# Kernel tuning notes

Hardware: AMD Instinct MI355X
Metric: run time of the kernel (lower is better)

## Reference

```python
import jax, jax.numpy as jnp
import numpy as np

MONOTONICITY = 1.0  # init kwarg monotonicity=1


def _interp_channel(xq, xs, ys):
    """Monotonic piecewise-linear interp for one channel.
    xq: (N,) query points; xs: (B,) sorted breakpoints; ys: (B,) knot values.
    Linear extrapolation beyond both ends using the edge segment slopes.
    """
    B = xs.shape[0]
    # segment index in [1, B-1]; elements below xs[0] / above xs[-1] use edge segments
    idx = jnp.clip(jnp.searchsorted(xs, xq), 1, B - 1)
    x0 = xs[idx - 1]
    x1 = xs[idx]
    y0 = ys[idx - 1]
    y1 = ys[idx]
    slope = (y1 - y0) / (x1 - x0)
    return y0 + slope * (xq - x0)


def setup_inputs() -> dict:
    key = jax.random.key(0)
    k1, k2, k3, k4 = jax.random.split(key, 4)
    N, C, B = 2097152, 16, 32
    x = jax.random.normal(k1, (N, C), dtype=jnp.float32)
    # learned parameters of MonoPointPWL (per channel)
    xp = jax.random.normal(k2, (C, B), dtype=jnp.float32)        # raw x positions (sorted at use)
    y0 = jax.random.normal(k3, (C,), dtype=jnp.float32)          # y value at first knot
    dy = jax.random.normal(k4, (C, B - 1), dtype=jnp.float32)    # raw segment deltas
    return {"x": x, "xp": xp, "y0": y0, "dy": dy}


def reference(x, xp, y0, dy):
    # sorted breakpoint x positions per channel: (C, B)
    xs = jnp.sort(xp, axis=1)
    # monotone knot values: y0 + cumsum(|dy|) * monotonicity, (C, B)
    steps = jnp.abs(dy) * MONOTONICITY
    ys = y0[:, None] + jnp.concatenate(
        [jnp.zeros_like(y0)[:, None], jnp.cumsum(steps, axis=1)], axis=1
    )
    # vectorize over channels: x is (N, C), params are (C, B)
    out = jax.vmap(_interp_channel, in_axes=(1, 0, 0), out_axes=1)(x, xs, ys)
    return out
```

## Files before the change

kernel.cpp:

```cpp
#include <hip/hip_runtime.h>
#include <hip/hip_bf16.h>


#define C_CH 16
#define B_KN 32
#define TAB_WORDS 12288


__global__ __launch_bounds__(512) void pwl_setup_kernel(
    const float* __restrict__ xp, const float* __restrict__ y0,
    const float* __restrict__ dy, float* __restrict__ ws) {
    __shared__ float s_x[C_CH][B_KN];
    __shared__ float s_xs[C_CH][B_KN];
    __shared__ float s_ys[C_CH][B_KN];
    int t = threadIdx.x;
    int c = t >> 5;
    int k = t & 31;
    float v = xp[c * B_KN + k];
    s_x[c][k] = v;
    __syncthreads();
    int rank = 0;
#pragma unroll
    for (int j = 0; j < B_KN; ++j) {
        float u = s_x[c][j];
        rank += (u < v || (u == v && j < k)) ? 1 : 0;
    }
    s_xs[c][rank] = v;
    float acc = y0[c];
    for (int j = 0; j < k; ++j) acc += fabsf(dy[c * (B_KN - 1) + j]);
    s_ys[c][k] = acc;
    __syncthreads();
    ws[c * B_KN + k] = s_xs[c][k];
    if (k < B_KN - 1) {
        float x0 = s_xs[c][k], x1 = s_xs[c][k + 1];
        float ya = s_ys[c][k], yb = s_ys[c][k + 1];
        float a = (yb - ya) / (x1 - x0);
        float b = ya - a * x0;
        ws[512 + c * B_KN + k]  = a;
        ws[1024 + c * B_KN + k] = b;
    } else {
        ws[512 + c * B_KN + k]  = 0.0f;
        ws[1024 + c * B_KN + k] = 0.0f;
    }
}

__global__ __launch_bounds__(512, 6) void pwl_main_kernel(
    const float4* __restrict__ x, float4* __restrict__ out,
    const float* __restrict__ ws, int n4) {
    __shared__ float s_tab[TAB_WORDS];
    int t = threadIdx.x;
    for (int w = t; w < TAB_WORDS; w += 512) {
        int bk = w & 31;
        int r  = w >> 5;
        int m  = r / 96;
        int tt = r - m * 96;
        int arr = tt >> 5;
        int idx = tt & 31;
        int c = ((bk & 3) << 2) + m;
        s_tab[w] = ws[arr * 512 + c * 32 + idx];
    }
    int c0 = (t & 3) << 2;
    float v15[4], v7[4], v23[4], v3[4], v11[4], v19[4], v27[4];
#pragma unroll
    for (int j = 0; j < 4; ++j) {
        const float* xs = ws + (c0 + j) * B_KN;
        v15[j] = xs[15];
        v7[j]  = xs[7];
        v23[j] = xs[23];
        v3[j]  = xs[3];
        v11[j] = xs[11];
        v19[j] = xs[19];
        v27[j] = xs[27];
    }
    __syncthreads();

    int bk = t & 31;
    int tid = blockIdx.x * 512 + t;
    int stride = gridDim.x * 512;

    int i = tid;
    if (i >= n4) return;
    float4 v = x[i];
    while (true) {
        int inext = i + stride;
        float4 vn = v;
        if (inext < n4) vn = x[inext];
        float xv[4] = {v.x, v.y, v.z, v.w};
        float r[4];
#pragma unroll
        for (int j = 0; j < 4; ++j) {
            float xq = xv[j];
            bool b16 = (v15[j] < xq);
            float l2v = b16 ? v23[j] : v7[j];
            bool b8 = (l2v < xq);
            float l3a = b16 ? v19[j] : v3[j];
            float l3b = b16 ? v27[j] : v11[j];
            float l3v = b8 ? l3b : l3a;
            bool b4 = (l3v < xq);
            int pos = (b16 ? 16 : 0) + (b8 ? 8 : 0) + (b4 ? 4 : 0);
            float w1 = s_tab[((j * 96 + (pos + 1)) << 5) | bk];
            pos += (w1 < xq) ? 2 : 0;
            float w2 = s_tab[((j * 96 + pos) << 5) | bk];
            pos += (w2 < xq) ? 1 : 0;
            int seg = pos < 2 ? 0 : (pos > 31 ? 30 : pos - 1);
            float a = s_tab[((j * 96 + 32 + seg) << 5) | bk];
            float b = s_tab[((j * 96 + 64 + seg) << 5) | bk];
            r[j] = fmaf(a, xq, b);
        }
        out[i] = make_float4(r[0], r[1], r[2], r[3]);
        if (inext >= n4) break;
        i = inext;
        v = vn;
    }
}

extern "C" void kernel_launch(void* const* d_in, const int* in_sizes, int n_in,
                              void* d_out, int out_size, void* d_ws, size_t ws_size,
                              hipStream_t stream) {
    const float* x  = (const float*)d_in[0];
    const float* xp = (const float*)d_in[1];
    const float* y0 = (const float*)d_in[2];
    const float* dy = (const float*)d_in[3];
    float* out = (float*)d_out;
    float* ws  = (float*)d_ws;

    pwl_setup_kernel<<<1, 512, 0, stream>>>(xp, y0, dy, ws);

    int n4 = in_sizes[0] / 4;
    int blocks = 768;
    pwl_main_kernel<<<blocks, 512, 0, stream>>>((const float4*)x, (float4*)out, ws, n4);
}
```

Measured before the change: 57.86 us.

## Shrink LDS table copies, process two float4 per iteration, nontemporal stores

Cuts the shared-memory lookup table from 32 to 16 interleaved copies, shrinking LDS per block so more blocks can be resident. The loop now loads two float4 values per iteration instead of software-prefetching one ahead, and writes results with nontemporal stores to avoid polluting cache. Grid size rises to 1024 blocks and the occupancy hint in launch bounds is dropped. Fewer copies can raise LDS bank conflicts on the table lookups.

Result: no change. 58.68 us (+1.4%).

```diff
diff --git a/kernel.cpp b/kernel.cpp
--- a/kernel.cpp
+++ b/kernel.cpp
@@ -4,7 +4,10 @@
 
 #define C_CH 16
 #define B_KN 32
-#define TAB_WORDS 12288
+#define COPIES 16
+#define TAB_WORDS (96 * 4 * COPIES)
+
+typedef float f4v __attribute__((ext_vector_type(4)));
 
 
 __global__ __launch_bounds__(512) void pwl_setup_kernel(
@@ -44,19 +47,19 @@
     }
 }
 
-__global__ __launch_bounds__(512, 6) void pwl_main_kernel(
+__global__ __launch_bounds__(512) void pwl_main_kernel(
     const float4* __restrict__ x, float4* __restrict__ out,
     const float* __restrict__ ws, int n4) {
     __shared__ float s_tab[TAB_WORDS];
     int t = threadIdx.x;
     for (int w = t; w < TAB_WORDS; w += 512) {
-        int bk = w & 31;
-        int r  = w >> 5;
+        int cp = w & 15;
+        int r  = w >> 4;
         int m  = r / 96;
         int tt = r - m * 96;
         int arr = tt >> 5;
         int idx = tt & 31;
-        int c = ((bk & 3) << 2) + m;
+        int c = ((cp & 3) << 2) + m;
         s_tab[w] = ws[arr * 512 + c * 32 + idx];
     }
     int c0 = (t & 3) << 2;
@@ -74,22 +77,20 @@
     }
     __syncthreads();
 
-    int bk = t & 31;
+    int cp = t & 15;
     int tid = blockIdx.x * 512 + t;
-    int stride = gridDim.x * 512;
+    int total = gridDim.x * 512;
 
-    int i = tid;
-    if (i >= n4) return;
-    float4 v = x[i];
-    while (true) {
-        int inext = i + stride;
-        float4 vn = v;
-        if (inext < n4) vn = x[inext];
-        float xv[4] = {v.x, v.y, v.z, v.w};
-        float r[4];
+    for (int i = tid; i < n4; i += 2 * total) {
+        int i1 = i + total;
+        float4 v0 = x[i];
+        float4 v1 = (i1 < n4) ? x[i1] : v0;
+        float xv[8] = {v0.x, v0.y, v0.z, v0.w, v1.x, v1.y, v1.z, v1.w};
+        float rr[8];
 #pragma unroll
-        for (int j = 0; j < 4; ++j) {
-            float xq = xv[j];
+        for (int u = 0; u < 8; ++u) {
+            int j = u & 3;
+            float xq = xv[u];
             bool b16 = (v15[j] < xq);
             float l2v = b16 ? v23[j] : v7[j];
             bool b8 = (l2v < xq);
@@ -98,19 +99,21 @@
             float l3v = b8 ? l3b : l3a;
             bool b4 = (l3v < xq);
             int pos = (b16 ? 16 : 0) + (b8 ? 8 : 0) + (b4 ? 4 : 0);
-            float w1 = s_tab[((j * 96 + (pos + 1)) << 5) | bk];
+            float w1 = s_tab[((j * 96 + (pos + 1)) << 4) | cp];
             pos += (w1 < xq) ? 2 : 0;
-            float w2 = s_tab[((j * 96 + pos) << 5) | bk];
+            float w2 = s_tab[((j * 96 + pos) << 4) | cp];
             pos += (w2 < xq) ? 1 : 0;
             int seg = pos < 2 ? 0 : (pos > 31 ? 30 : pos - 1);
-            float a = s_tab[((j * 96 + 32 + seg) << 5) | bk];
-            float b = s_tab[((j * 96 + 64 + seg) << 5) | bk];
-            r[j] = fmaf(a, xq, b);
+            float a = s_tab[((j * 96 + 32 + seg) << 4) | cp];
+            float b = s_tab[((j * 96 + 64 + seg) << 4) | cp];
+            rr[u] = fmaf(a, xq, b);
         }
-        out[i] = make_float4(r[0], r[1], r[2], r[3]);
-        if (inext >= n4) break;
-        i = inext;
-        v = vn;
+        f4v r0 = {rr[0], rr[1], rr[2], rr[3]};
+        __builtin_nontemporal_store(r0, (f4v*)&out[i]);
+        if (i1 < n4) {
+            f4v r1 = {rr[4], rr[5], rr[6], rr[7]};
+            __builtin_nontemporal_store(r1, (f4v*)&out[i1]);
+        }
     }
 }
 
@@ -127,6 +130,6 @@
     pwl_setup_kernel<<<1, 512, 0, stream>>>(xp, y0, dy, ws);
 
     int n4 = in_sizes[0] / 4;
-    int blocks = 768;
+    int blocks = 1024;
     pwl_main_kernel<<<blocks, 512, 0, stream>>>((const float4*)x, (float4*)out, ws, n4);
 }
```
